# Kernel tuning notes

Hardware: AMD Instinct MI355X
Metric: run time of the kernel (lower is better)

## Reference

```python
import jax, jax.numpy as jnp
import numpy as np

B, C, H, W = 8, 256, 48, 48
HW = H * W
DK = C // 8
LN_EPS = 1e-5


def setup_inputs() -> dict:
    key = jax.random.key(0)
    ks = jax.random.split(key, 16)
    s = lambda fan: 1.0 / np.sqrt(fan)
    return {
        "img_feat": jax.random.normal(ks[0], (B, C, H, W), jnp.float32),
        "text_feat": jax.random.normal(ks[1], (B, C), jnp.float32),
        "l": jax.random.normal(ks[2], (1, HW), jnp.float32),
        "Wg1": jax.random.normal(ks[3], (C, 2 * C), jnp.float32) * s(C),
        "bg1": jax.random.normal(ks[4], (2 * C,), jnp.float32) * 0.01,
        "ln_g": jnp.ones((2 * C,), jnp.float32),
        "ln_b": jnp.zeros((2 * C,), jnp.float32),
        "Wg2": jax.random.normal(ks[5], (2 * C, C), jnp.float32) * s(2 * C),
        "bg2": jax.random.normal(ks[6], (C,), jnp.float32) * 0.01,
        "Wq": jax.random.normal(ks[7], (DK, C), jnp.float32) * s(C),
        "bq": jax.random.normal(ks[8], (DK,), jnp.float32) * 0.01,
        "Wk": jax.random.normal(ks[9], (DK, C), jnp.float32) * s(C),
        "bk": jax.random.normal(ks[10], (DK,), jnp.float32) * 0.01,
        "Wv": jax.random.normal(ks[11], (C, C), jnp.float32) * s(C),
        "bv": jax.random.normal(ks[12], (C,), jnp.float32) * 0.01,
        "gamma": jax.random.normal(ks[13], (1,), jnp.float32) * 0.1,
    }


def reference(img_feat, text_feat, l, Wg1, bg1, ln_g, ln_b, Wg2, bg2,
              Wq, bq, Wk, bk, Wv, bv, gamma):
    b, c, h, w = img_feat.shape
    hw = h * w
    # G(text_feat): Linear -> LayerNorm -> GELU (exact) -> Linear
    t = text_feat @ Wg1 + bg1                          # [B, 2C]
    mu = jnp.mean(t, axis=-1, keepdims=True)
    var = jnp.mean((t - mu) ** 2, axis=-1, keepdims=True)
    t = (t - mu) / jnp.sqrt(var + LN_EPS) * ln_g + ln_b
    t = jax.nn.gelu(t, approximate=False)
    GvT = t @ Wg2 + bg2                                # [B, C]
    # F_T = GvT^T outer l  -> [B, C, HW]
    FT = GvT[:, :, None] * l.reshape(-1)[None, None, :]
    x = img_feat.reshape(b, c, hw)
    # 1x1 convs are channel matmuls
    Q = jnp.einsum('dc,bcn->bdn', Wq, x) + bq[None, :, None]   # [B, dk, HW]
    K = jnp.einsum('dc,bcn->bdn', Wk, FT) + bk[None, :, None]  # [B, dk, HW]
    V = jnp.einsum('dc,bcn->bdn', Wv, FT) + bv[None, :, None]  # [B, C, HW]
    # energy = Q^T K (NO 1/sqrt(d_k) scaling, as in the source)
    energy = jnp.einsum('bdi,bdj->bij', Q, K)                  # [B, HW, HW]
    attn = jax.nn.softmax(energy, axis=-1)
    out = jnp.einsum('bcj,bij->bci', V, attn).reshape(b, c, h, w)
    return img_feat + gamma.reshape(()) * out
```

## Files before the change

### kernel.cpp

```cpp
#include <hip/hip_runtime.h>
#include <math.h>

#define B_ 8
#define C_ 256
#define C2_ 512
#define DK_ 32
#define HW_ 2304

#define WS_WQ   0
#define WS_VG   2048
#define WS_QB   4096

__device__ __forceinline__ float gelu_exact(float x) {
    return 0.5f * x * (1.0f + erff(x * 0.70710678118654752f));
}

__global__ __launch_bounds__(512) void k_prep(
    const float* __restrict__ text,
    const float* __restrict__ Wg1,  const float* __restrict__ bg1,
    const float* __restrict__ ln_g, const float* __restrict__ ln_b,
    const float* __restrict__ Wg2,  const float* __restrict__ bg2,
    const float* __restrict__ Wq,   const float* __restrict__ bq,
    const float* __restrict__ Wk,   const float* __restrict__ Wv,
    float* __restrict__ ws)
{
    const int b = blockIdx.x >> 3;
    const int tile = blockIdx.x & 7;
    const int tid = threadIdx.x;

    __shared__ float tx[C_];
    __shared__ __align__(16) float tsh[C2_];
    __shared__ __align__(16) float gvs[C_];
    __shared__ float part2[2][C_];
    __shared__ float r1[8], r2[8];
    __shared__ float kg[DK_];

    if (tid < C_) tx[tid] = text[b * C_ + tid];
    __syncthreads();

    float acc = bg1[tid];
    #pragma unroll 8
    for (int c = 0; c < C_; ++c)
        acc += tx[c] * Wg1[(size_t)c * C2_ + tid];

    float s1 = acc, s2 = acc * acc;
    for (int o = 32; o; o >>= 1) {
        s1 += __shfl_down(s1, o);
        s2 += __shfl_down(s2, o);
    }
    if ((tid & 63) == 0) { r1[tid >> 6] = s1; r2[tid >> 6] = s2; }
    __syncthreads();
    s1 = 0.f; s2 = 0.f;
    #pragma unroll
    for (int u = 0; u < 8; ++u) { s1 += r1[u]; s2 += r2[u]; }
    const float mu = s1 * (1.0f / 512.0f);
    const float rstd = rsqrtf(s2 * (1.0f / 512.0f) - mu * mu + 1e-5f);
    tsh[tid] = gelu_exact((acc - mu) * rstd * ln_g[tid] + ln_b[tid]);
    __syncthreads();

    {
        const int col = tid & 255, half = tid >> 8;
        float g = 0.f;
        const float* wcol = Wg2 + (size_t)(half * 256) * C_ + col;
        #pragma unroll 8
        for (int j = 0; j < 256; ++j)
            g += tsh[half * 256 + j] * wcol[(size_t)j * C_];
        part2[half][col] = g;
    }
    __syncthreads();
    if (tid < C_) gvs[tid] = part2[0][tid] + part2[1][tid] + bg2[tid];
    __syncthreads();

    const int o = tid >> 4, sub = tid & 15;
    const float4* gv4 = (const float4*)gvs + sub * 4;
    {
        const float4* wrow = (const float4*)(Wv + (size_t)(tile * 32 + o) * C_) + sub * 4;
        float a = 0.f;
        #pragma unroll
        for (int k4 = 0; k4 < 4; ++k4) {
            float4 w4 = wrow[k4], g4 = gv4[k4];
            a += w4.x * g4.x + w4.y * g4.y + w4.z * g4.z + w4.w * g4.w;
        }
        a += __shfl_xor(a, 1);
        a += __shfl_xor(a, 2);
        a += __shfl_xor(a, 4);
        a += __shfl_xor(a, 8);
        if (sub == 0) ws[WS_VG + b * C_ + tile * 32 + o] = a;
    }

    if (tile == 0) {
        const float4* wrow = (const float4*)(Wk + (size_t)o * C_) + sub * 4;
        float a = 0.f;
        #pragma unroll
        for (int k4 = 0; k4 < 4; ++k4) {
            float4 w4 = wrow[k4], g4 = gv4[k4];
            a += w4.x * g4.x + w4.y * g4.y + w4.z * g4.z + w4.w * g4.w;
        }
        a += __shfl_xor(a, 1);
        a += __shfl_xor(a, 2);
        a += __shfl_xor(a, 4);
        a += __shfl_xor(a, 8);
        if (sub == 0) kg[o] = a;
        __syncthreads();
        if (tid < C_) {
            float w = 0.f;
            #pragma unroll
            for (int d = 0; d < DK_; ++d) w += kg[d] * Wq[(size_t)d * C_ + tid];
            ws[WS_WQ + b * C_ + tid] = w;
        }
        if (tid == 0) {
            float q = 0.f;
            #pragma unroll
            for (int d = 0; d < DK_; ++d) q += kg[d] * bq[d];
            ws[WS_QB + b] = q;
        }
    }
}

__global__ __launch_bounds__(256) void k_fused(
    const float* __restrict__ img, const float* __restrict__ l,
    const float* __restrict__ bv,  const float* __restrict__ gamma,
    const float* __restrict__ ws,  float* __restrict__ out)
{
    const int blk = blockIdx.x;
    const int b = blk / 72;
    const int i0 = (blk % 72) * 32;
    const int tid = threadIdx.x;

    __shared__ float lsh[HW_];
    __shared__ float tile[C_][32];
    __shared__ float wq[C_], vgb[C_], bvs[C_];
    __shared__ float part[8][32];
    __shared__ float aa[32], ss[32];
    __shared__ float redmn[4], redmx[4];

    wq[tid]  = ws[WS_WQ + b * C_ + tid];
    vgb[tid] = ws[WS_VG + b * C_ + tid];
    bvs[tid] = bv[tid];
    float mn = 1e30f, mx = -1e30f;
    #pragma unroll
    for (int j = tid; j < HW_; j += 256) {
        float v = l[j];
        lsh[j] = v;
        mn = fminf(mn, v); mx = fmaxf(mx, v);
    }
    for (int o = 32; o; o >>= 1) {
        mn = fminf(mn, __shfl_down(mn, o));
        mx = fmaxf(mx, __shfl_down(mx, o));
    }
    if ((tid & 63) == 0) { redmn[tid >> 6] = mn; redmx[tid >> 6] = mx; }
    __syncthreads();
    const float lmin = fminf(fminf(redmn[0], redmn[1]), fminf(redmn[2], redmn[3]));
    const float lmax = fmaxf(fmaxf(redmx[0], redmx[1]), fmaxf(redmx[2], redmx[3]));

    const int pix = tid & 31, sub = tid >> 5;
    {
        const float* x = img + ((size_t)b * C_ + sub * 32) * HW_ + i0 + pix;
        float acc = 0.f;
        #pragma unroll 8
        for (int k = 0; k < 32; ++k) {
            float v = x[(size_t)k * HW_];
            tile[sub * 32 + k][pix] = v;
            acc += wq[sub * 32 + k] * v;
        }
        part[sub][pix] = acc;
    }
    __syncthreads();
    if (tid < 32) {
        float a = ws[WS_QB + b];
        #pragma unroll
        for (int u = 0; u < 8; ++u) a += part[u][tid];
        aa[tid] = a;
    }
    __syncthreads();

    {
        const int spix = tid >> 3, ssub = tid & 7;
        const float m = aa[spix];
        const float mxv = (m >= 0.f) ? m * lmax : m * lmin;
        float se = 0.f, sle = 0.f;
        #pragma unroll 4
        for (int j = ssub; j < HW_; j += 8) {
            float lj = lsh[j];
            float e = __expf(m * lj - mxv);
            se += e;
            sle += e * lj;
        }
        se += __shfl_xor(se, 1);  sle += __shfl_xor(sle, 1);
        se += __shfl_xor(se, 2);  sle += __shfl_xor(sle, 2);
        se += __shfl_xor(se, 4);  sle += __shfl_xor(sle, 4);
        if (ssub == 0) ss[spix] = sle / se;
    }
    __syncthreads();

    {
        const float g = gamma[0];
        const float s = ss[pix];
        float* o = out + ((size_t)b * C_ + sub * 32) * HW_ + i0 + pix;
        #pragma unroll 8
        for (int k = 0; k < 32; ++k) {
            const int c = sub * 32 + k;
            o[(size_t)k * HW_] = tile[c][pix] + g * (vgb[c] * s + bvs[c]);
        }
    }
}

extern "C" void kernel_launch(void* const* d_in, const int* in_sizes, int n_in,
                              void* d_out, int out_size, void* d_ws, size_t ws_size,
                              hipStream_t stream) {
    const float* img   = (const float*)d_in[0];
    const float* text  = (const float*)d_in[1];
    const float* l     = (const float*)d_in[2];
    const float* Wg1   = (const float*)d_in[3];
    const float* bg1   = (const float*)d_in[4];
    const float* ln_g  = (const float*)d_in[5];
    const float* ln_b  = (const float*)d_in[6];
    const float* Wg2   = (const float*)d_in[7];
    const float* bg2   = (const float*)d_in[8];
    const float* Wq    = (const float*)d_in[9];
    const float* bq    = (const float*)d_in[10];
    const float* Wk    = (const float*)d_in[11];
    const float* Wv    = (const float*)d_in[13];
    const float* bv    = (const float*)d_in[14];
    const float* gamma = (const float*)d_in[15];
    float* out = (float*)d_out;
    float* ws  = (float*)d_ws;

    k_prep<<<64, 512, 0, stream>>>(text, Wg1, bg1, ln_g, ln_b, Wg2, bg2,
                                   Wq, bq, Wk, Wv, ws);
    k_fused<<<576, 256, 0, stream>>>(img, l, bv, gamma, ws, out);
}
```

Measured before the change: 52.47 us.

## Merge prep and fused kernels into one cooperative launch with grid sync

Replaces the two launches with a single cooperative kernel. The first 64 blocks compute the text-branch projections while the other 576 blocks load the l vector and their image tiles into shared memory at the same time. A grid-wide sync then lets the image blocks read the projected weights and finish the softmax-reduced output. This aims to hide the prep kernel's latency and the launch gap behind the image loads, at the cost of a grid barrier and a limit on co-resident blocks. If the cooperative launch fails, it falls back to the original two-kernel path.

```diff
diff --git a/kernel.cpp b/kernel.cpp
--- a/kernel.cpp
+++ b/kernel.cpp
@@ -1,5 +1,8 @@
 #include <hip/hip_runtime.h>
+#include <hip/hip_cooperative_groups.h>
 #include <math.h>
+
+namespace cg = cooperative_groups;
 
 #define B_ 8
 #define C_ 256
@@ -10,6 +13,8 @@
 #define WS_WQ   0
 #define WS_VG   2048
 #define WS_QB   4096
+
+#define NPREP 64
 
 __device__ __forceinline__ float gelu_exact(float x) {
     return 0.5f * x * (1.0f + erff(x * 0.70710678118654752f));
@@ -163,6 +168,199 @@
             tile[sub * 32 + k][pix] = v;
             acc += wq[sub * 32 + k] * v;
         }
+        part[sub][pix] = acc;
+    }
+    __syncthreads();
+    if (tid < 32) {
+        float a = ws[WS_QB + b];
+        #pragma unroll
+        for (int u = 0; u < 8; ++u) a += part[u][tid];
+        aa[tid] = a;
+    }
+    __syncthreads();
+
+    {
+        const int spix = tid >> 3, ssub = tid & 7;
+        const float m = aa[spix];
+        const float mxv = (m >= 0.f) ? m * lmax : m * lmin;
+        float se = 0.f, sle = 0.f;
+        #pragma unroll 4
+        for (int j = ssub; j < HW_; j += 8) {
+            float lj = lsh[j];
+            float e = __expf(m * lj - mxv);
+            se += e;
+            sle += e * lj;
+        }
+        se += __shfl_xor(se, 1);  sle += __shfl_xor(sle, 1);
+        se += __shfl_xor(se, 2);  sle += __shfl_xor(sle, 2);
+        se += __shfl_xor(se, 4);  sle += __shfl_xor(sle, 4);
+        if (ssub == 0) ss[spix] = sle / se;
+    }
+    __syncthreads();
+
+    {
+        const float g = gamma[0];
+        const float s = ss[pix];
+        float* o = out + ((size_t)b * C_ + sub * 32) * HW_ + i0 + pix;
+        #pragma unroll 8
+        for (int k = 0; k < 32; ++k) {
+            const int c = sub * 32 + k;
+            o[(size_t)k * HW_] = tile[c][pix] + g * (vgb[c] * s + bvs[c]);
+        }
+    }
+}
+
+__global__ __launch_bounds__(256) void k_all(
+    const float* __restrict__ img,  const float* __restrict__ text,
+    const float* __restrict__ l,
+    const float* __restrict__ Wg1,  const float* __restrict__ bg1,
+    const float* __restrict__ ln_g, const float* __restrict__ ln_b,
+    const float* __restrict__ Wg2,  const float* __restrict__ bg2,
+    const float* __restrict__ Wq,   const float* __restrict__ bq,
+    const float* __restrict__ Wk,   const float* __restrict__ Wv,
+    const float* __restrict__ bv,   const float* __restrict__ gamma,
+    float* __restrict__ ws,         float* __restrict__ out)
+{
+    const int blk = blockIdx.x;
+    const int tid = threadIdx.x;
+
+    __shared__ __align__(16) float lsh[HW_];
+    __shared__ float tile[C_][32];
+    __shared__ float wq[C_], vgb[C_], bvs[C_];
+    __shared__ float part[8][32];
+    __shared__ float aa[32], ss[32];
+    __shared__ float redmn[4], redmx[4];
+
+    float lmin = 0.f, lmax = 0.f;
+    int b = 0, i0 = 0, pix = 0, sub = 0;
+
+    if (blk < NPREP) {
+        const int pb = blk >> 3;
+        const int tile8 = blk & 7;
+        float* tx  = lsh;
+        float* tsh = lsh + 256;
+        float* gvs = lsh + 768;
+        float* r1  = lsh + 1536;
+        float* r2  = lsh + 1544;
+        float* kg  = lsh + 1552;
+
+        tx[tid] = text[pb * C_ + tid];
+        __syncthreads();
+
+        float a0 = bg1[tid], a1 = bg1[tid + 256];
+        #pragma unroll 8
+        for (int c = 0; c < C_; ++c) {
+            float t = tx[c];
+            a0 += t * Wg1[(size_t)c * C2_ + tid];
+            a1 += t * Wg1[(size_t)c * C2_ + tid + 256];
+        }
+        float s1 = a0 + a1, s2 = a0 * a0 + a1 * a1;
+        for (int o = 32; o; o >>= 1) {
+            s1 += __shfl_down(s1, o);
+            s2 += __shfl_down(s2, o);
+        }
+        if ((tid & 63) == 0) { r1[tid >> 6] = s1; r2[tid >> 6] = s2; }
+        __syncthreads();
+        s1 = r1[0] + r1[1] + r1[2] + r1[3];
+        s2 = r2[0] + r2[1] + r2[2] + r2[3];
+        const float mu = s1 * (1.0f / 512.0f);
+        const float rstd = rsqrtf(s2 * (1.0f / 512.0f) - mu * mu + 1e-5f);
+        float g0 = gelu_exact((a0 - mu) * rstd * ln_g[tid] + ln_b[tid]);
+        float g1 = gelu_exact((a1 - mu) * rstd * ln_g[tid + 256] + ln_b[tid + 256]);
+        __syncthreads();
+        tsh[tid] = g0; tsh[tid + 256] = g1;
+        __syncthreads();
+
+        float g = bg2[tid];
+        #pragma unroll 8
+        for (int j = 0; j < C2_; ++j)
+            g += tsh[j] * Wg2[(size_t)j * C_ + tid];
+        gvs[tid] = g;
+        __syncthreads();
+
+        const int o = tid >> 3, su = tid & 7;
+        const float4* gv4 = (const float4*)gvs + su * 8;
+        {
+            const float4* wrow = (const float4*)(Wv + (size_t)(tile8 * 32 + o) * C_) + su * 8;
+            float a = 0.f;
+            #pragma unroll
+            for (int k4 = 0; k4 < 8; ++k4) {
+                float4 w4 = wrow[k4], q4 = gv4[k4];
+                a += w4.x * q4.x + w4.y * q4.y + w4.z * q4.z + w4.w * q4.w;
+            }
+            a += __shfl_xor(a, 1);
+            a += __shfl_xor(a, 2);
+            a += __shfl_xor(a, 4);
+            if (su == 0) ws[WS_VG + pb * C_ + tile8 * 32 + o] = a;
+        }
+        if (tile8 == 0) {
+            const float4* wrow = (const float4*)(Wk + (size_t)o * C_) + su * 8;
+            float a = 0.f;
+            #pragma unroll
+            for (int k4 = 0; k4 < 8; ++k4) {
+                float4 w4 = wrow[k4], q4 = gv4[k4];
+                a += w4.x * q4.x + w4.y * q4.y + w4.z * q4.z + w4.w * q4.w;
+            }
+            a += __shfl_xor(a, 1);
+            a += __shfl_xor(a, 2);
+            a += __shfl_xor(a, 4);
+            if (su == 0) kg[o] = a;
+            __syncthreads();
+            float w = 0.f;
+            #pragma unroll
+            for (int d = 0; d < DK_; ++d) w += kg[d] * Wq[(size_t)d * C_ + tid];
+            ws[WS_WQ + pb * C_ + tid] = w;
+            if (tid == 0) {
+                float q = 0.f;
+                #pragma unroll
+                for (int d = 0; d < DK_; ++d) q += kg[d] * bq[d];
+                ws[WS_QB + pb] = q;
+            }
+        }
+        __threadfence();
+    } else {
+        const int idx = blk - NPREP;
+        b = idx / 72;
+        i0 = (idx % 72) * 32;
+        pix = tid & 31; sub = tid >> 5;
+
+        bvs[tid] = bv[tid];
+        float mn = 1e30f, mx = -1e30f;
+        #pragma unroll
+        for (int j = tid; j < HW_; j += 256) {
+            float v = l[j];
+            lsh[j] = v;
+            mn = fminf(mn, v); mx = fmaxf(mx, v);
+        }
+        for (int o = 32; o; o >>= 1) {
+            mn = fminf(mn, __shfl_down(mn, o));
+            mx = fmaxf(mx, __shfl_down(mx, o));
+        }
+        if ((tid & 63) == 0) { redmn[tid >> 6] = mn; redmx[tid >> 6] = mx; }
+
+        {
+            const float* x = img + ((size_t)b * C_ + sub * 32) * HW_ + i0 + pix;
+            #pragma unroll 8
+            for (int k = 0; k < 32; ++k)
+                tile[sub * 32 + k][pix] = x[(size_t)k * HW_];
+        }
+        __syncthreads();
+        lmin = fminf(fminf(redmn[0], redmn[1]), fminf(redmn[2], redmn[3]));
+        lmax = fmaxf(fmaxf(redmx[0], redmx[1]), fmaxf(redmx[2], redmx[3]));
+    }
+
+    cg::this_grid().sync();
+    if (blk < NPREP) return;
+
+    wq[tid]  = ws[WS_WQ + b * C_ + tid];
+    vgb[tid] = ws[WS_VG + b * C_ + tid];
+    __syncthreads();
+
+    {
+        float acc = 0.f;
+        #pragma unroll 8
+        for (int k = 0; k < 32; ++k)
+            acc += wq[sub * 32 + k] * tile[sub * 32 + k][pix];
         part[sub][pix] = acc;
     }
     __syncthreads();
@@ -226,7 +424,20 @@
     float* out = (float*)d_out;
     float* ws  = (float*)d_ws;
 
-    k_prep<<<64, 512, 0, stream>>>(text, Wg1, bg1, ln_g, ln_b, Wg2, bg2,
-                                   Wq, bq, Wk, Wv, ws);
-    k_fused<<<576, 256, 0, stream>>>(img, l, bv, gamma, ws, out);
+    void* args[] = {
+        (void*)&img, (void*)&text, (void*)&l,
+        (void*)&Wg1, (void*)&bg1, (void*)&ln_g, (void*)&ln_b,
+        (void*)&Wg2, (void*)&bg2, (void*)&Wq, (void*)&bq,
+        (void*)&Wk, (void*)&Wv, (void*)&bv, (void*)&gamma,
+        (void*)&ws, (void*)&out
+    };
+    hipError_t err = hipLaunchCooperativeKernel((const void*)k_all,
+                                                dim3(NPREP + 576), dim3(256),
+                                                args, 0, stream);
+    if (err != hipSuccess) {
+        (void)hipGetLastError();
+        k_prep<<<64, 512, 0, stream>>>(text, Wg1, bg1, ln_g, ln_b, Wg2, bg2,
+                                       Wq, bq, Wk, Wv, ws);
+        k_fused<<<576, 256, 0, stream>>>(img, l, bv, gamma, ws, out);
+    }
 }
```

New measurement: 130.8 us. +149.4%, slower.

## Keep image tile in registers with float4 loads instead of shared memory

Applied to the files above, without the earlier changes.

The fused kernel now loads the 256x32 image tile as float4 vectors into per-thread registers, where it previously staged scalar loads through a 32 KB shared tile. The registers are reused for both the Q projection and the final residual write. The image loads are issued before the barrier so they overlap the l min/max reduction, and gamma is folded into the per-channel scale and bias. This cuts shared memory use and widens global accesses, at the cost of 32 extra registers per thread and a larger 32-way partial reduction.

```diff
diff --git a/kernel.cpp b/kernel.cpp
--- a/kernel.cpp
+++ b/kernel.cpp
@@ -127,49 +127,65 @@
     const int i0 = (blk % 72) * 32;
     const int tid = threadIdx.x;
 
-    __shared__ float lsh[HW_];
-    __shared__ float tile[C_][32];
-    __shared__ float wq[C_], vgb[C_], bvs[C_];
-    __shared__ float part[8][32];
+    __shared__ __align__(16) float lsh[HW_];
+    __shared__ float wq[C_], Asc[C_], Bsc[C_];
+    __shared__ float part[32][36];
     __shared__ float aa[32], ss[32];
     __shared__ float redmn[4], redmx[4];
 
+    const float g = gamma[0];
     wq[tid]  = ws[WS_WQ + b * C_ + tid];
-    vgb[tid] = ws[WS_VG + b * C_ + tid];
-    bvs[tid] = bv[tid];
+    Asc[tid] = g * ws[WS_VG + b * C_ + tid];
+    Bsc[tid] = g * bv[tid];
+
     float mn = 1e30f, mx = -1e30f;
-    #pragma unroll
-    for (int j = tid; j < HW_; j += 256) {
-        float v = l[j];
-        lsh[j] = v;
-        mn = fminf(mn, v); mx = fmaxf(mx, v);
+    {
+        const float4* l4 = (const float4*)l;
+        for (int j = tid; j < HW_ / 4; j += 256) {
+            float4 v = l4[j];
+            ((float4*)lsh)[j] = v;
+            mn = fminf(mn, fminf(fminf(v.x, v.y), fminf(v.z, v.w)));
+            mx = fmaxf(mx, fmaxf(fmaxf(v.x, v.y), fmaxf(v.z, v.w)));
+        }
     }
     for (int o = 32; o; o >>= 1) {
         mn = fminf(mn, __shfl_down(mn, o));
         mx = fmaxf(mx, __shfl_down(mx, o));
     }
     if ((tid & 63) == 0) { redmn[tid >> 6] = mn; redmx[tid >> 6] = mx; }
-    __syncthreads();
+
+    const int p4 = tid & 7, cl = tid >> 3;
+    const float4* img4 = (const float4*)(img + (size_t)b * C_ * HW_ + i0);
+    float4 cache[8];
+    #pragma unroll
+    for (int k = 0; k < 8; ++k)
+        cache[k] = img4[(size_t)(k * 32 + cl) * (HW_ / 4) + p4];
+
+    __syncthreads();
+
+    {
+        float4 pa = make_float4(0.f, 0.f, 0.f, 0.f);
+        #pragma unroll
+        for (int k = 0; k < 8; ++k) {
+            const float w = wq[k * 32 + cl];
+            pa.x = fmaf(w, cache[k].x, pa.x);
+            pa.y = fmaf(w, cache[k].y, pa.y);
+            pa.z = fmaf(w, cache[k].z, pa.z);
+            pa.w = fmaf(w, cache[k].w, pa.w);
+        }
+        part[cl][p4 * 4 + 0] = pa.x;
+        part[cl][p4 * 4 + 1] = pa.y;
+        part[cl][p4 * 4 + 2] = pa.z;
+        part[cl][p4 * 4 + 3] = pa.w;
+    }
     const float lmin = fminf(fminf(redmn[0], redmn[1]), fminf(redmn[2], redmn[3]));
     const float lmax = fmaxf(fmaxf(redmx[0], redmx[1]), fmaxf(redmx[2], redmx[3]));
-
-    const int pix = tid & 31, sub = tid >> 5;
-    {
-        const float* x = img + ((size_t)b * C_ + sub * 32) * HW_ + i0 + pix;
-        float acc = 0.f;
-        #pragma unroll 8
-        for (int k = 0; k < 32; ++k) {
-            float v = x[(size_t)k * HW_];
-            tile[sub * 32 + k][pix] = v;
-            acc += wq[sub * 32 + k] * v;
-        }
-        part[sub][pix] = acc;
-    }
-    __syncthreads();
+    __syncthreads();
+
     if (tid < 32) {
         float a = ws[WS_QB + b];
-        #pragma unroll
-        for (int u = 0; u < 8; ++u) a += part[u][tid];
+        #pragma unroll 8
+        for (int u = 0; u < 32; ++u) a += part[u][tid];
         aa[tid] = a;
     }
     __syncthreads();
@@ -182,9 +198,9 @@
         #pragma unroll 4
         for (int j = ssub; j < HW_; j += 8) {
             float lj = lsh[j];
-            float e = __expf(m * lj - mxv);
+            float e = __expf(fmaf(m, lj, -mxv));
             se += e;
-            sle += e * lj;
+            sle = fmaf(e, lj, sle);
         }
         se += __shfl_xor(se, 1);  sle += __shfl_xor(sle, 1);
         se += __shfl_xor(se, 2);  sle += __shfl_xor(sle, 2);
@@ -194,13 +210,19 @@
     __syncthreads();
 
     {
-        const float g = gamma[0];
-        const float s = ss[pix];
-        float* o = out + ((size_t)b * C_ + sub * 32) * HW_ + i0 + pix;
-        #pragma unroll 8
-        for (int k = 0; k < 32; ++k) {
-            const int c = sub * 32 + k;
-            o[(size_t)k * HW_] = tile[c][pix] + g * (vgb[c] * s + bvs[c]);
+        const float4 s4 = make_float4(ss[p4 * 4 + 0], ss[p4 * 4 + 1],
+                                      ss[p4 * 4 + 2], ss[p4 * 4 + 3]);
+        float4* out4 = (float4*)(out + (size_t)b * C_ * HW_ + i0);
+        #pragma unroll
+        for (int k = 0; k < 8; ++k) {
+            const int c = k * 32 + cl;
+            const float A = Asc[c], Bc = Bsc[c];
+            float4 v = cache[k], o;
+            o.x = v.x + fmaf(A, s4.x, Bc);
+            o.y = v.y + fmaf(A, s4.y, Bc);
+            o.z = v.z + fmaf(A, s4.z, Bc);
+            o.w = v.w + fmaf(A, s4.w, Bc);
+            out4[(size_t)c * (HW_ / 4) + p4] = o;
         }
     }
 }
```

Result: faster. 47.36 us (-9.7%).
